# Kernel optimization log

Hardware: AMD Instinct MI355X
Metric: run time of the kernel (lower is better)

## Reference

```python
import jax, jax.numpy as jnp
import numpy as np

EMB = 512
HEADS = 8
HD = EMB // HEADS
DEPTH = 6
CONT = 100
CAT_DIMS = [100] * 28
CAT = len(CAT_DIMS)
HID = int(EMB * (4.0 / 3.0))  # 682, FT-Transformer ReGLU hidden
B = 128
OFFSETS = jnp.asarray(np.concatenate([[0], np.cumsum(CAT_DIMS[:-1])]).astype(np.int32))
SQRT_EMB = float(np.sqrt(EMB))  # scores are DIVIDED by emb**-0.5 in the source


def setup_inputs() -> dict:
    key = jax.random.key(0)
    ks = jax.random.split(key, 16)
    s = 0.02
    x_cat = jax.random.randint(ks[0], (B, CAT), 0, CAT_DIMS[0]).astype(jnp.float32)
    x_cont = jax.random.normal(ks[1], (B, CONT), dtype=jnp.float32)
    x = jnp.concatenate([x_cat, x_cont], axis=1)  # [B, CAT+CONT]
    return {
        "x": x,
        "tok_w": jax.random.normal(ks[2], (CONT + 1, EMB)) * s,
        "tok_b": jax.random.normal(ks[3], (CONT + CAT, EMB)) * s,
        "cat_emb": jax.random.normal(ks[4], (sum(CAT_DIMS), EMB)) * s,
        "Wqkv": jax.random.normal(ks[5], (DEPTH, EMB, 3 * EMB)) * s,
        "bqkv": jnp.zeros((DEPTH, 3 * EMB)),
        "Wout": jax.random.normal(ks[6], (DEPTH, EMB, EMB)) * s,
        "bout": jnp.zeros((DEPTH, EMB)),
        "W0": jax.random.normal(ks[7], (DEPTH, EMB, 2 * HID)) * s,
        "b0": jnp.zeros((DEPTH, 2 * HID)),
        "W1": jax.random.normal(ks[8], (DEPTH, HID, EMB)) * s,
        "b1": jnp.zeros((DEPTH, EMB)),
        "ln0_g": jnp.ones((DEPTH, EMB)),
        "ln0_b": jnp.zeros((DEPTH, EMB)),
        "ln1_g": jnp.ones((DEPTH, EMB)),
        "ln1_b": jnp.zeros((DEPTH, EMB)),
    }


def _ln(x, g, b):
    m = x.mean(-1, keepdims=True)
    v = x.var(-1, keepdims=True)
    return (x - m) / jnp.sqrt(v + 1e-5) * g + b


def _attn(x, Wqkv, bqkv, Wout, bout):
    Bn, S, _ = x.shape
    # faithful layout: reshape to (B,S,H,3*hd), move heads, chunk last dim
    qkv = (x @ Wqkv + bqkv).reshape(Bn, S, HEADS, 3 * HD).transpose(0, 2, 1, 3)
    q, k, v = jnp.split(qkv, 3, axis=-1)  # each [B,H,S,hd]
    scores = jnp.einsum("bhqd,bhkd->bhqk", q, k) * SQRT_EMB  # / (emb**-0.5)
    attn = jax.nn.softmax(jax.nn.softmax(scores, axis=-1), axis=-1)  # double softmax, as in source
    o = jnp.einsum("bhqk,bhkd->bhqd", attn, v)
    o = o.transpose(0, 2, 1, 3).reshape(Bn, S, EMB)
    return o @ Wout + bout


def _reglu(x):
    a, b = jnp.split(x, 2, axis=-1)
    return a * jax.nn.relu(b)


def _forward(x, tok_w, tok_b, cat_emb, Wqkv, bqkv, Wout, bout, W0, b0, W1, b1,
             ln0_g, ln0_b, ln1_g, ln1_b):
    # --- feature tokenizer ---
    x_cats = x[:, :CAT].astype(jnp.int32)
    x_conts = jnp.concatenate([jnp.ones((x.shape[0], 1), x.dtype), x[:, CAT:]], axis=1)  # [B, CONT+1]
    h = tok_w[None] * x_conts[:, :, None]  # [B, CONT+1, EMB]
    h = jnp.concatenate([h, cat_emb[x_cats + OFFSETS[None]]], axis=1)  # [B, S=129, EMB]
    bias = jnp.concatenate([jnp.zeros((1, EMB), h.dtype), tok_b], axis=0)
    h = h + bias[None]
    # --- transformer stack ---
    for i in range(DEPTH):
        xin = _ln(h, ln0_g[i], ln0_b[i]) if i else h  # layer 0 has no norm0
        h = h + _attn(xin, Wqkv[i], bqkv[i], Wout[i], bout[i])
        r = _ln(h, ln1_g[i], ln1_b[i])
        r = _reglu(r @ W0[i] + b0[i]) @ W1[i] + b1[i]
        h = h + r
    return h[:, 0]  # CLS token


def reference(x, tok_w, tok_b, cat_emb, Wqkv, bqkv, Wout, bout, W0, b0, W1, b1,
              ln0_g, ln0_b, ln1_g, ln1_b):
    return _forward(x, tok_w, tok_b, cat_emb, Wqkv, bqkv, Wout, bout, W0, b0, W1, b1,
                    ln0_g, ln0_b, ln1_g, ln1_b)
```

## Files before the change

### kernel.cpp

```cpp
#include <hip/hip_runtime.h>
#include <hip/hip_bf16.h>
#include <stdint.h>


typedef __hip_bfloat16 bf16_t;
typedef __attribute__((ext_vector_type(8))) __bf16 bf16x8;
typedef __attribute__((ext_vector_type(4))) __bf16 bf16x4;
typedef __attribute__((ext_vector_type(2))) __bf16 bf16x2;
typedef __attribute__((ext_vector_type(4))) float floatx4;

constexpr int M_ROWS = 16512;
constexpr float SQRT_EMB_F = 22.627416997969522f;

__device__ __forceinline__ floatx4 mfma16(bf16x8 a, bf16x8 b, floatx4 c) {
  return __builtin_amdgcn_mfma_f32_16x16x32_bf16(a, b, c, 0, 0, 0);
}

__device__ __forceinline__ void gload_lds16(const bf16_t* g, bf16_t* l) {
  __builtin_amdgcn_global_load_lds(
      (const __attribute__((address_space(1))) void*)g,
      (__attribute__((address_space(3))) void*)l, 16, 0, 0);
}

__device__ __forceinline__ size_t frag_chunk(int m, int k, int KT) {
  return ((size_t)(m >> 4) * KT + (k >> 5)) * 512 + (m & 15) * 8 + 128 * ((k >> 3) & 3);
}
__device__ __forceinline__ size_t frag_elem(int m, int k, int KT) {
  return frag_chunk(m, k, KT) + (k & 7);
}

template <int PERM>
__global__ __launch_bounds__(256) void transpose_cvt(const float* __restrict__ W,
    bf16_t* __restrict__ WT, int K, int N, int KP, int NP)
{
  __shared__ float tile[32][33];
  int k0 = blockIdx.x * 32, n0 = blockIdx.y * 32;
  const float* Wl = W + (size_t)blockIdx.z * K * N;
  bf16_t* WTl = WT + (size_t)blockIdx.z * NP * KP;
  const int KT = KP >> 5;
  #pragma unroll
  for (int r = 0; r < 32; r += 8) {
    int k = k0 + threadIdx.y + r, n = n0 + threadIdx.x;
    int srcn = PERM ? ((n & 1) ? 682 + (n >> 1) : (n >> 1)) : n;
    int valid = (k < K) && (PERM ? (n < 1364) : (n < N));
    tile[threadIdx.y + r][threadIdx.x] = valid ? Wl[(size_t)k * N + srcn] : 0.f;
  }
  __syncthreads();
  #pragma unroll
  for (int r = 0; r < 32; r += 8) {
    int n = n0 + threadIdx.y + r, k = k0 + threadIdx.x;
    if (n < NP && k < KP)
      WTl[frag_elem(n, k, KT)] = __float2bfloat16(tile[threadIdx.x][threadIdx.y + r]);
  }
}

__global__ __launch_bounds__(256) void tokenizer_kernel(const float* __restrict__ x,
    const float* __restrict__ tok_w, const float* __restrict__ tok_b,
    const float* __restrict__ cat_emb, float* __restrict__ h, bf16_t* __restrict__ ab)
{
  int row = blockIdx.x * 4 + (threadIdx.x >> 6);
  int lane = threadIdx.x & 63, e0 = lane * 8;
  int b = row / 129, t = row - b * 129;
  float v[8];
  if (t == 0) {
    #pragma unroll
    for (int u = 0; u < 8; u++) v[u] = tok_w[e0 + u];
  } else if (t <= 100) {
    float xv = x[(size_t)b * 128 + 28 + (t - 1)];
    const float* wp = tok_w + (size_t)t * 512 + e0;
    const float* bp = tok_b + (size_t)(t - 1) * 512 + e0;
    #pragma unroll
    for (int u = 0; u < 8; u++) v[u] = wp[u] * xv + bp[u];
  } else {
    int j = t - 101;
    int idx = (int)x[(size_t)b * 128 + j] + 100 * j;
    const float* cp = cat_emb + (size_t)idx * 512 + e0;
    const float* bp = tok_b + (size_t)(t - 1) * 512 + e0;
    #pragma unroll
    for (int u = 0; u < 8; u++) v[u] = cp[u] + bp[u];
  }
  float* hr = h + (size_t)row * 512 + e0;
  #pragma unroll
  for (int u = 0; u < 8; u++) hr[u] = v[u];
  bf16x8 o8;
  #pragma unroll
  for (int u = 0; u < 8; u++) o8[u] = (__bf16)__float2bfloat16(v[u]);
  *(bf16x8*)(ab + ((size_t)(row >> 4) * 16 + (lane >> 2)) * 512 + (row & 15) * 8 + 128 * (lane & 3)) = o8;
}

template <int MODE>
__global__ __launch_bounds__(256, 4) void gemm_frag(const bf16_t* __restrict__ A,
    const bf16_t* __restrict__ BT, const float* __restrict__ bias, int biasN,
    const float* __restrict__ resid, void* __restrict__ outp, int K, int N)
{
  __shared__ bf16_t lsB[2][8][512];

  const int total = gridDim.x * gridDim.y;
  const int lin = blockIdx.y * gridDim.x + blockIdx.x;
  const int xcd = lin & 7, kb2 = lin >> 3;
  const int qch = total >> 3, rch = total & 7;
  const int idx = xcd * qch + (xcd < rch ? xcd : rch) + kb2;
  const int bm = idx / gridDim.x;
  const int bn = idx - bm * gridDim.x;
  const int m0 = bm * 128, n0 = bn * 128;

  const int tid = threadIdx.x;
  const int w = tid >> 6, l = tid & 63, l15 = l & 15, quad = l >> 4;
  const int wm = (w >> 1) * 64, wn = (w & 1) * 64;
  const int KT = K >> 5;

  const bf16_t* pa[4];
  #pragma unroll
  for (int i = 0; i < 4; i++)
    pa[i] = A + ((size_t)((m0 >> 4) + (w >> 1) * 4 + i) * KT) * 512 + l * 8;

  const bf16_t* gB0 = BT + ((size_t)((n0 >> 4) + 2 * w) * KT) * 512 + l * 8;
  const bf16_t* gB1 = gB0 + (size_t)KT * 512;
  const int sb = w * 2;
  const int rb = (w & 1) * 4;

  auto stageB = [&](int buf, int t) {
    const size_t go = (size_t)t * 512;
    gload_lds16(gB0 + go, &lsB[buf][sb][0]);
    gload_lds16(gB1 + go, &lsB[buf][sb + 1][0]);
  };

  floatx4 z4 = {0.f, 0.f, 0.f, 0.f};
  floatx4 acc[4][4];
  #pragma unroll
  for (int i = 0; i < 4; i++)
    #pragma unroll
    for (int j = 0; j < 4; j++) acc[i][j] = z4;

  bf16x8 af[4];
  #pragma unroll
  for (int i = 0; i < 4; i++) af[i] = *(const bf16x8*)pa[i];
  stageB(0, 0);
  __syncthreads();

  int cur = 0;
  for (int t = 0; t < KT; ++t) {
    if (t + 1 < KT) stageB(cur ^ 1, t + 1);
    bf16x8 bg[4];
    #pragma unroll
    for (int j = 0; j < 4; j++) bg[j] = *(const bf16x8*)&lsB[cur][rb + j][l * 8];
    #pragma unroll
    for (int i = 0; i < 4; i++) {
      #pragma unroll
      for (int j = 0; j < 4; j++)
        acc[i][j] = mfma16(bg[j], af[i], acc[i][j]);
      if (t + 1 < KT)
        af[i] = *(const bf16x8*)(pa[i] + (size_t)(t + 1) * 512);
    }
    __syncthreads();
    cur ^= 1;
  }

  #pragma unroll
  for (int i = 0; i < 4; i++) {
    int m = m0 + wm + i * 16 + l15;
    #pragma unroll
    for (int j = 0; j < 4; j++) {
      int nb = n0 + wn + j * 16 + quad * 4;
      if (MODE == 2) {
        int c2b = nb >> 1;
        bf16x2 o2;
        #pragma unroll
        for (int u = 0; u < 2; u++) {
          int c2 = c2b + u;
          bool vld = (2 * c2 < biasN);
          float av = acc[i][j][2 * u]     + (vld ? bias[c2] : 0.f);
          float bv = acc[i][j][2 * u + 1] + (vld ? bias[682 + c2] : 0.f);
          o2[u] = (__bf16)__float2bfloat16(av * fmaxf(bv, 0.f));
        }
        *(bf16x2*)&((bf16_t*)outp)[frag_elem(m, c2b, (N >> 1) >> 5)] = o2;
      } else {
        bf16x4 o4;
        #pragma unroll
        for (int r = 0; r < 4; r++) {
          float bv = (nb + r < biasN) ? bias[nb + r] : 0.f;
          o4[r] = (__bf16)__float2bfloat16(acc[i][j][r] + bv);
        }
        *(bf16x4*)&((bf16_t*)outp)[frag_elem(m, nb, N >> 5)] = o4;
      }
    }
  }
  (void)resid;
}

template <int DOLN, int DOOUT>
__global__ __launch_bounds__(512, 4) void gemm_ln(const bf16_t* __restrict__ A,
    const bf16_t* __restrict__ BT, const float* __restrict__ bias,
    const float* __restrict__ resid, float* __restrict__ hout,
    const float* __restrict__ g, const float* __restrict__ beta,
    bf16_t* __restrict__ ab, float* __restrict__ outp, int K)
{
  __shared__ float lnred[2][8][32];

  const int nwg = gridDim.x;
  const int lin = blockIdx.x;
  const int xcd = lin & 7, kb2 = lin >> 3;
  const int qch = nwg >> 3, rch = nwg & 7;
  const int idx = xcd * qch + (xcd < rch ? xcd : rch) + kb2;
  const int m0 = idx * 32;

  const int tid = threadIdx.x;
  const int w = tid >> 6, l = tid & 63, l15 = l & 15, quad = l >> 4;
  const int wn = w * 64;
  const int KT = K >> 5;

  const bf16_t* pa0 = A + ((size_t)(m0 >> 4) * KT) * 512 + l * 8;
  const bf16_t* pa1 = pa0 + (size_t)KT * 512;
  const bf16_t* pb[4];
  #pragma unroll
  for (int j = 0; j < 4; j++)
    pb[j] = BT + ((size_t)((wn >> 4) + j) * KT) * 512 + l * 8;

  floatx4 acc[2][4];
  #pragma unroll
  for (int i = 0; i < 2; i++)
    #pragma unroll
    for (int j = 0; j < 4; j++) acc[i][j] = floatx4{0.f, 0.f, 0.f, 0.f};

  bf16x8 af0 = *(const bf16x8*)pa0;
  bf16x8 af1 = *(const bf16x8*)pa1;
  bf16x8 bg[4];
  #pragma unroll
  for (int j = 0; j < 4; j++) bg[j] = *(const bf16x8*)pb[j];

  for (int t = 0; t < KT; ++t) {
    #pragma unroll
    for (int j = 0; j < 4; j++) {
      acc[0][j] = mfma16(bg[j], af0, acc[0][j]);
      acc[1][j] = mfma16(bg[j], af1, acc[1][j]);
      if (t + 1 < KT) bg[j] = *(const bf16x8*)(pb[j] + (size_t)(t + 1) * 512);
    }
    if (t + 1 < KT) {
      af0 = *(const bf16x8*)(pa0 + (size_t)(t + 1) * 512);
      af1 = *(const bf16x8*)(pa1 + (size_t)(t + 1) * 512);
    }
  }

  const int colb = wn + quad * 4;
  float s[2] = {0.f, 0.f}, q[2] = {0.f, 0.f};
  #pragma unroll
  for (int i = 0; i < 2; i++) {
    const int m = m0 + i * 16 + l15;
    float* hr = hout + (size_t)m * 512;
    const float* rr = resid + (size_t)m * 512;
    #pragma unroll
    for (int j = 0; j < 4; j++) {
      const int nb = colb + j * 16;
      float4 rv = *(const float4*)(rr + nb);
      float4 bv = *(const float4*)(bias + nb);
      floatx4 hv;
      hv[0] = acc[i][j][0] + bv.x + rv.x;
      hv[1] = acc[i][j][1] + bv.y + rv.y;
      hv[2] = acc[i][j][2] + bv.z + rv.z;
      hv[3] = acc[i][j][3] + bv.w + rv.w;
      acc[i][j] = hv;
      float4 hw = {hv[0], hv[1], hv[2], hv[3]};
      *(float4*)(hr + nb) = hw;
      if (DOOUT) {
        if (m % 129 == 0)
          *(float4*)(outp + (size_t)(m / 129) * 512 + nb) = hw;
      }
      s[i] += hv[0] + hv[1] + hv[2] + hv[3];
      q[i] += hv[0] * hv[0] + hv[1] * hv[1] + hv[2] * hv[2] + hv[3] * hv[3];
    }
  }

  if (DOLN) {
    #pragma unroll
    for (int i = 0; i < 2; i++) {
      s[i] += __shfl_xor(s[i], 16); s[i] += __shfl_xor(s[i], 32);
      q[i] += __shfl_xor(q[i], 16); q[i] += __shfl_xor(q[i], 32);
    }
    if (quad == 0) {
      lnred[0][w][l15]      = s[0];  lnred[1][w][l15]      = q[0];
      lnred[0][w][16 + l15] = s[1];  lnred[1][w][16 + l15] = q[1];
    }
    __syncthreads();
    #pragma unroll
    for (int i = 0; i < 2; i++) {
      const int m = m0 + i * 16 + l15;
      float ss = 0.f, qq = 0.f;
      #pragma unroll
      for (int wv = 0; wv < 8; wv++) {
        ss += lnred[0][wv][i * 16 + l15];
        qq += lnred[1][wv][i * 16 + l15];
      }
      float mean = ss * (1.f / 512.f);
      float var = qq * (1.f / 512.f) - mean * mean;
      float rstd = rsqrtf(var + 1e-5f);
      #pragma unroll
      for (int j = 0; j < 4; j++) {
        const int nb = colb + j * 16;
        float4 gg = *(const float4*)(g + nb);
        float4 bb = *(const float4*)(beta + nb);
        bf16x4 o4;
        o4[0] = (__bf16)__float2bfloat16((acc[i][j][0] - mean) * rstd * gg.x + bb.x);
        o4[1] = (__bf16)__float2bfloat16((acc[i][j][1] - mean) * rstd * gg.y + bb.y);
        o4[2] = (__bf16)__float2bfloat16((acc[i][j][2] - mean) * rstd * gg.z + bb.z);
        o4[3] = (__bf16)__float2bfloat16((acc[i][j][3] - mean) * rstd * gg.w + bb.w);
        *(bf16x4*)&ab[frag_elem(m, nb, 16)] = o4;
      }
    }
  }
}

constexpr int SP = 160;
__global__ __launch_bounds__(256) void attn_kernel(const bf16_t* __restrict__ qkv,
                                                   bf16_t* __restrict__ attnout)
{
  __shared__ bf16_t vt_lds[64 * SP];
  __shared__ float sc[32 * SP];
  bf16_t* p_lds = (bf16_t*)sc;
  __bf16* vt_raw = (__bf16*)vt_lds;

  const int bh = blockIdx.x, b = bh >> 3, hh = bh & 7;
  const int tid = threadIdx.x;
  const int w = tid >> 6, l = tid & 63, l15 = l & 15, quad = l >> 4;
  const int rbase = b * 129;

  for (int i = tid; i < SP * 64 / 2; i += 256) ((unsigned int*)vt_lds)[i] = 0u;
  __syncthreads();
  for (int c = tid; c < 129 * 8; c += 256) {
    int s = c >> 3, ch = c & 7;
    bf16x8 tv = *(const bf16x8*)(qkv + frag_chunk(rbase + s, hh * 192 + 128 + ch * 8, 48));
    #pragma unroll
    for (int j = 0; j < 8; j++) vt_raw[(size_t)(ch * 8 + j) * SP + s] = tv[j];
  }
  __syncthreads();

  for (int qt = 0; qt < 5; qt++) {
    bf16x8 zq = {};
    bf16x8 aq[2][2];
    #pragma unroll
    for (int mt = 0; mt < 2; mt++) {
      int m = qt * 32 + mt * 16 + l15;
      #pragma unroll
      for (int t = 0; t < 2; t++)
        aq[mt][t] = (m < 129)
            ? *(const bf16x8*)(qkv + frag_chunk(rbase + m, hh * 192 + t * 32 + quad * 8, 48)) : zq;
    }
    for (int nt = w; nt < 10; nt += 4) {
      int krow = nt * 16 + l15;
      floatx4 a0 = {0.f, 0.f, 0.f, 0.f}, a1 = {0.f, 0.f, 0.f, 0.f};
      #pragma unroll
      for (int t = 0; t < 2; t++) {
        bf16x8 kf = (krow < 129)
            ? *(const bf16x8*)(qkv + frag_chunk(rbase + krow, hh * 192 + 64 + t * 32 + quad * 8, 48))
            : zq;
        a0 = mfma16(aq[0][t], kf, a0);
        a1 = mfma16(aq[1][t], kf, a1);
      }
      #pragma unroll
      for (int r = 0; r < 4; r++) {
        sc[(quad * 4 + r) * SP + nt * 16 + l15]      = a0[r] * SQRT_EMB_F;
        sc[(16 + quad * 4 + r) * SP + nt * 16 + l15] = a1[r] * SQRT_EMB_F;
      }
    }
    __syncthreads();

    {
      int row = tid >> 3, sub = tid & 7;
      float vv[20];
      float mx = -1e30f;
      #pragma unroll
      for (int c = 0; c < 20; c++) {
        int j = sub + c * 8;
        vv[c] = (j < 129) ? sc[row * SP + j] : -1e30f;
        mx = fmaxf(mx, vv[c]);
      }
      #pragma unroll
      for (int o = 1; o < 8; o <<= 1) mx = fmaxf(mx, __shfl_xor(mx, o, 8));
      float sum = 0.f;
      #pragma unroll
      for (int c = 0; c < 20; c++) {
        int j = sub + c * 8;
        vv[c] = (j < 129) ? __expf(vv[c] - mx) : 0.f;
        sum += vv[c];
      }
      #pragma unroll
      for (int o = 1; o < 8; o <<= 1) sum += __shfl_xor(sum, o, 8);
      float inv = 1.f / sum;
      float mx2 = 0.f;
      #pragma unroll
      for (int c = 0; c < 20; c++) { vv[c] *= inv; mx2 = fmaxf(mx2, vv[c]); }
      #pragma unroll
      for (int o = 1; o < 8; o <<= 1) mx2 = fmaxf(mx2, __shfl_xor(mx2, o, 8));
      float sum2 = 0.f;
      #pragma unroll
      for (int c = 0; c < 20; c++) {
        int j = sub + c * 8;
        vv[c] = (j < 129) ? __expf(vv[c] - mx2) : 0.f;
        sum2 += vv[c];
      }
      #pragma unroll
      for (int o = 1; o < 8; o <<= 1) sum2 += __shfl_xor(sum2, o, 8);
      float inv2 = 1.f / sum2;
      __syncthreads();
      #pragma unroll
      for (int c = 0; c < 20; c++) {
        int j = sub + c * 8;
        p_lds[row * SP + j] = __float2bfloat16(vv[c] * inv2);
      }
    }
    __syncthreads();

    {
      int mt = w >> 1, nt0 = (w & 1) * 2;
      floatx4 oacc[2];
      oacc[0] = floatx4{0.f, 0.f, 0.f, 0.f};
      oacc[1] = floatx4{0.f, 0.f, 0.f, 0.f};
      #pragma unroll
      for (int t = 0; t < 5; t++) {
        bf16x8 pf = *(const bf16x8*)&p_lds[(mt * 16 + l15) * SP + t * 32 + quad * 8];
        #pragma unroll
        for (int n = 0; n < 2; n++) {
          bf16x8 vf = *(const bf16x8*)&vt_lds[((nt0 + n) * 16 + l15) * SP + t * 32 + quad * 8];
          oacc[n] = mfma16(pf, vf, oacc[n]);
        }
      }
      #pragma unroll
      for (int n = 0; n < 2; n++)
        #pragma unroll
        for (int r = 0; r < 4; r++) {
          int sq = qt * 32 + mt * 16 + quad * 4 + r;
          if (sq < 129) {
            int cc = hh * 64 + (nt0 + n) * 16 + l15;
            attnout[frag_elem(rbase + sq, cc, 16)] = __float2bfloat16(oacc[n][r]);
          }
        }
    }
    __syncthreads();
  }
}

extern "C" void kernel_launch(void* const* d_in, const int* in_sizes, int n_in,
                              void* d_out, int out_size, void* d_ws, size_t ws_size,
                              hipStream_t stream)
{
  const float* x       = (const float*)d_in[0];
  const float* tok_w   = (const float*)d_in[1];
  const float* tok_b   = (const float*)d_in[2];
  const float* cat_emb = (const float*)d_in[3];
  const float* Wqkv    = (const float*)d_in[4];
  const float* bqkv    = (const float*)d_in[5];
  const float* Wout    = (const float*)d_in[6];
  const float* bout    = (const float*)d_in[7];
  const float* W0      = (const float*)d_in[8];
  const float* b0      = (const float*)d_in[9];
  const float* W1      = (const float*)d_in[10];
  const float* b1      = (const float*)d_in[11];
  const float* ln0_g   = (const float*)d_in[12];
  const float* ln0_b   = (const float*)d_in[13];
  const float* ln1_g   = (const float*)d_in[14];
  const float* ln1_b   = (const float*)d_in[15];

  size_t off = 0;
  char* base = (char*)d_ws;
  auto alloc = [&](size_t n) { char* p = base + off; off += (n + 255) & ~(size_t)255; return p; };
  float*  h     = (float*) alloc((size_t)M_ROWS * 512 * 4);
  bf16_t* ab    = (bf16_t*)alloc((size_t)M_ROWS * 512 * 2);
  bf16_t* qkv   = (bf16_t*)alloc((size_t)M_ROWS * 1536 * 2);
  bf16_t* attno = (bf16_t*)alloc((size_t)M_ROWS * 512 * 2);
  bf16_t* regl  = (bf16_t*)alloc((size_t)M_ROWS * 704 * 2);
  bf16_t* WqkvT = (bf16_t*)alloc((size_t)6 * 1536 * 512 * 2);
  bf16_t* WoutT = (bf16_t*)alloc((size_t)6 * 512 * 512 * 2);
  bf16_t* W0T   = (bf16_t*)alloc((size_t)6 * 1408 * 512 * 2);
  bf16_t* W1T   = (bf16_t*)alloc((size_t)6 * 512 * 704 * 2);
  (void)ws_size; (void)in_sizes; (void)n_in; (void)out_size;

  dim3 tb(32, 8, 1);
  transpose_cvt<0><<<dim3(16, 48, 6), tb, 0, stream>>>(Wqkv, WqkvT, 512, 1536, 512, 1536);
  transpose_cvt<0><<<dim3(16, 16, 6), tb, 0, stream>>>(Wout, WoutT, 512, 512, 512, 512);
  transpose_cvt<1><<<dim3(16, 44, 6), tb, 0, stream>>>(W0, W0T, 512, 1364, 512, 1408);
  transpose_cvt<0><<<dim3(22, 16, 6), tb, 0, stream>>>(W1, W1T, 682, 512, 704, 512);

  tokenizer_kernel<<<M_ROWS / 4, 256, 0, stream>>>(x, tok_w, tok_b, cat_emb, h, ab);

  const int GLN = M_ROWS / 32;
  for (int i = 0; i < 6; i++) {
    gemm_frag<0><<<dim3(12, 129), 256, 0, stream>>>(
        ab, WqkvT + (size_t)i * 1536 * 512, bqkv + (size_t)i * 1536, 1536, nullptr, qkv, 512, 1536);
    attn_kernel<<<1024, 256, 0, stream>>>(qkv, attno);
    gemm_ln<1, 0><<<GLN, 512, 0, stream>>>(
        attno, WoutT + (size_t)i * 512 * 512, bout + (size_t)i * 512, h, h,
        ln1_g + (size_t)i * 512, ln1_b + (size_t)i * 512, ab, nullptr, 512);
    gemm_frag<2><<<dim3(11, 129), 256, 0, stream>>>(
        ab, W0T + (size_t)i * 1408 * 512, b0 + (size_t)i * 1364, 1364, nullptr, regl, 512, 1408);
    if (i < 5)
      gemm_ln<1, 0><<<GLN, 512, 0, stream>>>(
          regl, W1T + (size_t)i * 512 * 704, b1 + (size_t)i * 512, h, h,
          ln0_g + (size_t)(i + 1) * 512, ln0_b + (size_t)(i + 1) * 512, ab, nullptr, 704);
    else
      gemm_ln<0, 1><<<GLN, 512, 0, stream>>>(
          regl, W1T + (size_t)i * 512 * 704, b1 + (size_t)i * 512, h, h,
          nullptr, nullptr, nullptr, (float*)d_out, 704);
  }
}
```

Baseline: 1.305 ms.

## Stage A tiles through LDS in GEMMs and double gemm_ln row tile

gemm_frag now stages A fragments through double-buffered LDS with async global-to-LDS loads instead of reading A directly from global memory per wave. gemm_ln is restructured to stage both A and B through LDS and covers 64 rows per block instead of 32, halving the number of blocks and reusing each B tile across more rows. The final layer skips writing h since only the CLS output is needed. This aims to cut redundant global loads at the cost of more LDS use, fewer workgroups for gemm_ln (258), and extra barriers.

```diff
diff --git a/kernel.cpp b/kernel.cpp
--- a/kernel.cpp
+++ b/kernel.cpp
@@ -91,8 +91,9 @@
 template <int MODE>
 __global__ __launch_bounds__(256, 4) void gemm_frag(const bf16_t* __restrict__ A,
     const bf16_t* __restrict__ BT, const float* __restrict__ bias, int biasN,
-    const float* __restrict__ resid, void* __restrict__ outp, int K, int N)
+    void* __restrict__ outp, int K, int N)
 {
+  __shared__ bf16_t lsA[2][8][512];
   __shared__ bf16_t lsB[2][8][512];
 
   const int total = gridDim.x * gridDim.y;
@@ -109,20 +110,20 @@
   const int wm = (w >> 1) * 64, wn = (w & 1) * 64;
   const int KT = K >> 5;
 
-  const bf16_t* pa[4];
-  #pragma unroll
-  for (int i = 0; i < 4; i++)
-    pa[i] = A + ((size_t)((m0 >> 4) + (w >> 1) * 4 + i) * KT) * 512 + l * 8;
-
+  const bf16_t* gA0 = A  + ((size_t)((m0 >> 4) + 2 * w) * KT) * 512 + l * 8;
+  const bf16_t* gA1 = gA0 + (size_t)KT * 512;
   const bf16_t* gB0 = BT + ((size_t)((n0 >> 4) + 2 * w) * KT) * 512 + l * 8;
   const bf16_t* gB1 = gB0 + (size_t)KT * 512;
-  const int sb = w * 2;
+  const int sa = w * 2;
+  const int ra = (w >> 1) * 4;
   const int rb = (w & 1) * 4;
 
-  auto stageB = [&](int buf, int t) {
+  auto stage = [&](int buf, int t) {
     const size_t go = (size_t)t * 512;
-    gload_lds16(gB0 + go, &lsB[buf][sb][0]);
-    gload_lds16(gB1 + go, &lsB[buf][sb + 1][0]);
+    gload_lds16(gA0 + go, &lsA[buf][sa][0]);
+    gload_lds16(gA1 + go, &lsA[buf][sa + 1][0]);
+    gload_lds16(gB0 + go, &lsB[buf][sa][0]);
+    gload_lds16(gB1 + go, &lsB[buf][sa + 1][0]);
   };
 
   floatx4 z4 = {0.f, 0.f, 0.f, 0.f};
@@ -132,26 +133,23 @@
     #pragma unroll
     for (int j = 0; j < 4; j++) acc[i][j] = z4;
 
-  bf16x8 af[4];
-  #pragma unroll
-  for (int i = 0; i < 4; i++) af[i] = *(const bf16x8*)pa[i];
-  stageB(0, 0);
+  stage(0, 0);
   __syncthreads();
 
   int cur = 0;
   for (int t = 0; t < KT; ++t) {
-    if (t + 1 < KT) stageB(cur ^ 1, t + 1);
-    bf16x8 bg[4];
-    #pragma unroll
-    for (int j = 0; j < 4; j++) bg[j] = *(const bf16x8*)&lsB[cur][rb + j][l * 8];
+    if (t + 1 < KT) stage(cur ^ 1, t + 1);
+    bf16x8 af[4], bg[4];
     #pragma unroll
     for (int i = 0; i < 4; i++) {
+      af[i] = *(const bf16x8*)&lsA[cur][ra + i][l * 8];
+      bg[i] = *(const bf16x8*)&lsB[cur][rb + i][l * 8];
+    }
+    #pragma unroll
+    for (int i = 0; i < 4; i++)
       #pragma unroll
       for (int j = 0; j < 4; j++)
         acc[i][j] = mfma16(bg[j], af[i], acc[i][j]);
-      if (t + 1 < KT)
-        af[i] = *(const bf16x8*)(pa[i] + (size_t)(t + 1) * 512);
-    }
     __syncthreads();
     cur ^= 1;
   }
@@ -185,7 +183,6 @@
       }
     }
   }
-  (void)resid;
 }
 
 template <int DOLN, int DOOUT>
@@ -195,59 +192,68 @@
     const float* __restrict__ g, const float* __restrict__ beta,
     bf16_t* __restrict__ ab, float* __restrict__ outp, int K)
 {
-  __shared__ float lnred[2][8][32];
+  __shared__ bf16_t lsA[2][4][512];
+  __shared__ bf16_t lsB[2][32][512];
+  __shared__ float lnred[2][8][64];
 
   const int nwg = gridDim.x;
   const int lin = blockIdx.x;
   const int xcd = lin & 7, kb2 = lin >> 3;
   const int qch = nwg >> 3, rch = nwg & 7;
   const int idx = xcd * qch + (xcd < rch ? xcd : rch) + kb2;
-  const int m0 = idx * 32;
+  const int m0 = idx * 64;
 
   const int tid = threadIdx.x;
   const int w = tid >> 6, l = tid & 63, l15 = l & 15, quad = l >> 4;
   const int wn = w * 64;
   const int KT = K >> 5;
 
-  const bf16_t* pa0 = A + ((size_t)(m0 >> 4) * KT) * 512 + l * 8;
-  const bf16_t* pa1 = pa0 + (size_t)KT * 512;
-  const bf16_t* pb[4];
-  #pragma unroll
-  for (int j = 0; j < 4; j++)
-    pb[j] = BT + ((size_t)((wn >> 4) + j) * KT) * 512 + l * 8;
-
-  floatx4 acc[2][4];
-  #pragma unroll
-  for (int i = 0; i < 2; i++)
+  const bf16_t* gB[4];
+  #pragma unroll
+  for (int s = 0; s < 4; s++)
+    gB[s] = BT + ((size_t)(4 * w + s) * KT) * 512 + l * 8;
+  const bf16_t* gA = A + ((size_t)((m0 >> 4) + (w & 3)) * KT) * 512 + l * 8;
+
+  auto stage = [&](int buf, int t) {
+    const size_t go = (size_t)t * 512;
+    #pragma unroll
+    for (int s = 0; s < 4; s++) gload_lds16(gB[s] + go, &lsB[buf][4 * w + s][0]);
+    if (w < 4) gload_lds16(gA + go, &lsA[buf][w][0]);
+  };
+
+  floatx4 acc[4][4];
+  #pragma unroll
+  for (int i = 0; i < 4; i++)
     #pragma unroll
     for (int j = 0; j < 4; j++) acc[i][j] = floatx4{0.f, 0.f, 0.f, 0.f};
 
-  bf16x8 af0 = *(const bf16x8*)pa0;
-  bf16x8 af1 = *(const bf16x8*)pa1;
-  bf16x8 bg[4];
-  #pragma unroll
-  for (int j = 0; j < 4; j++) bg[j] = *(const bf16x8*)pb[j];
-
+  stage(0, 0);
+  __syncthreads();
+
+  int cur = 0;
   for (int t = 0; t < KT; ++t) {
-    #pragma unroll
-    for (int j = 0; j < 4; j++) {
-      acc[0][j] = mfma16(bg[j], af0, acc[0][j]);
-      acc[1][j] = mfma16(bg[j], af1, acc[1][j]);
-      if (t + 1 < KT) bg[j] = *(const bf16x8*)(pb[j] + (size_t)(t + 1) * 512);
-    }
-    if (t + 1 < KT) {
-      af0 = *(const bf16x8*)(pa0 + (size_t)(t + 1) * 512);
-      af1 = *(const bf16x8*)(pa1 + (size_t)(t + 1) * 512);
-    }
+    if (t + 1 < KT) stage(cur ^ 1, t + 1);
+    bf16x8 af[4], bg[4];
+    #pragma unroll
+    for (int i = 0; i < 4; i++) af[i] = *(const bf16x8*)&lsA[cur][i][l * 8];
+    #pragma unroll
+    for (int j = 0; j < 4; j++) bg[j] = *(const bf16x8*)&lsB[cur][w * 4 + j][l * 8];
+    #pragma unroll
+    for (int i = 0; i < 4; i++)
+      #pragma unroll
+      for (int j = 0; j < 4; j++)
+        acc[i][j] = mfma16(bg[j], af[i], acc[i][j]);
+    __syncthreads();
+    cur ^= 1;
   }
 
   const int colb = wn + quad * 4;
-  float s[2] = {0.f, 0.f}, q[2] = {0.f, 0.f};
-  #pragma unroll
-  for (int i = 0; i < 2; i++) {
+  float s[4], q[4];
+  #pragma unroll
+  for (int i = 0; i < 4; i++) {
     const int m = m0 + i * 16 + l15;
-    float* hr = hout + (size_t)m * 512;
     const float* rr = resid + (size_t)m * 512;
+    s[i] = 0.f; q[i] = 0.f;
     #pragma unroll
     for (int j = 0; j < 4; j++) {
       const int nb = colb + j * 16;
@@ -260,7 +266,7 @@
       hv[3] = acc[i][j][3] + bv.w + rv.w;
       acc[i][j] = hv;
       float4 hw = {hv[0], hv[1], hv[2], hv[3]};
-      *(float4*)(hr + nb) = hw;
+      if (!DOOUT) *(float4*)(hout + (size_t)m * 512 + nb) = hw;
       if (DOOUT) {
         if (m % 129 == 0)
           *(float4*)(outp + (size_t)(m / 129) * 512 + nb) = hw;
@@ -272,17 +278,20 @@
 
   if (DOLN) {
     #pragma unroll
-    for (int i = 0; i < 2; i++) {
+    for (int i = 0; i < 4; i++) {
       s[i] += __shfl_xor(s[i], 16); s[i] += __shfl_xor(s[i], 32);
       q[i] += __shfl_xor(q[i], 16); q[i] += __shfl_xor(q[i], 32);
     }
     if (quad == 0) {
-      lnred[0][w][l15]      = s[0];  lnred[1][w][l15]      = q[0];
-      lnred[0][w][16 + l15] = s[1];  lnred[1][w][16 + l15] = q[1];
+      #pragma unroll
+      for (int i = 0; i < 4; i++) {
+        lnred[0][w][i * 16 + l15] = s[i];
+        lnred[1][w][i * 16 + l15] = q[i];
+      }
     }
     __syncthreads();
     #pragma unroll
-    for (int i = 0; i < 2; i++) {
+    for (int i = 0; i < 4; i++) {
       const int m = m0 + i * 16 + l15;
       float ss = 0.f, qq = 0.f;
       #pragma unroll
@@ -481,16 +490,16 @@
 
   tokenizer_kernel<<<M_ROWS / 4, 256, 0, stream>>>(x, tok_w, tok_b, cat_emb, h, ab);
 
-  const int GLN = M_ROWS / 32;
+  const int GLN = M_ROWS / 64;
   for (int i = 0; i < 6; i++) {
     gemm_frag<0><<<dim3(12, 129), 256, 0, stream>>>(
-        ab, WqkvT + (size_t)i * 1536 * 512, bqkv + (size_t)i * 1536, 1536, nullptr, qkv, 512, 1536);
+        ab, WqkvT + (size_t)i * 1536 * 512, bqkv + (size_t)i * 1536, 1536, qkv, 512, 1536);
     attn_kernel<<<1024, 256, 0, stream>>>(qkv, attno);
     gemm_ln<1, 0><<<GLN, 512, 0, stream>>>(
         attno, WoutT + (size_t)i * 512 * 512, bout + (size_t)i * 512, h, h,
         ln1_g + (size_t)i * 512, ln1_b + (size_t)i * 512, ab, nullptr, 512);
     gemm_frag<2><<<dim3(11, 129), 256, 0, stream>>>(
-        ab, W0T + (size_t)i * 1408 * 512, b0 + (size_t)i * 1364, 1364, nullptr, regl, 512, 1408);
+        ab, W0T + (size_t)i * 1408 * 512, b0 + (size_t)i * 1364, 1364, regl, 512, 1408);
     if (i < 5)
       gemm_ln<1, 0><<<GLN, 512, 0, stream>>>(
           regl, W1T + (size_t)i * 512 * 704, b1 + (size_t)i * 512, h, h,
```

Result: no change. 1.296 ms (-0.7%).
